# Performance work log

Measured on AMD Instinct MI355X. Metric: run time of the kernel, lower is better.

Reference implementation:

```python
import jax, jax.numpy as jnp
import numpy as np

N_NODES = 100000
N_EDGES = 1600000
IN_CH = 6
EDGE_FEAT = 8


def glorot(key, shape):
    lim = np.sqrt(6.0 / (shape[0] + shape[1]))
    return jax.random.uniform(key, shape, jnp.float32, -lim, lim)


def setup_inputs() -> dict:
    key = jax.random.key(0)
    ks = jax.random.split(key, 10)
    x = jax.random.normal(ks[0], (N_NODES, IN_CH), jnp.float32)
    edge_index = jax.random.randint(ks[1], (2, N_EDGES), 0, N_NODES, jnp.int64)
    edge_attr = jax.random.normal(ks[2], (N_EDGES, EDGE_FEAT), jnp.float32)
    return {
        "x": x,
        "edge_index": edge_index,
        "edge_attr": edge_attr,
        "W1": glorot(ks[3], (IN_CH, 32)), "b1": jnp.zeros((32,), jnp.float32),
        "W2": glorot(ks[4], (32, 16)), "b2": jnp.zeros((16,), jnp.float32),
        "W3": glorot(ks[5], (16 * 2 + EDGE_FEAT, 32)), "b3": jnp.zeros((32,), jnp.float32),
        "W4": glorot(ks[6], (32, 1)), "b4": jnp.zeros((1,), jnp.float32),
    }


def gcn_conv(x, src, dst, W, b, n_nodes):
    # PyG GCNConv: add self-loops, symmetric deg^{-1/2} normalization,
    # linear transform, scatter-add aggregation over incoming edges, bias.
    h = x @ W  # [N, out]
    deg = jnp.zeros((n_nodes,), h.dtype).at[dst].add(1.0) + 1.0  # +1 self-loop
    dinv = jax.lax.rsqrt(deg)  # [N]
    norm = dinv[src] * dinv[dst]  # [E]
    msg = h[src] * norm[:, None]  # gather + scale
    agg = jnp.zeros_like(h).at[dst].add(msg)
    agg = agg + h * (dinv * dinv)[:, None]  # self-loop term
    return agg + b


def reference(x, edge_index, edge_attr, W1, b1, W2, b2, W3, b3, W4, b4):
    src, dst = edge_index[0], edge_index[1]
    n = x.shape[0]
    h = jax.nn.relu(gcn_conv(x, src, dst, W1, b1, n))
    h = jax.nn.relu(gcn_conv(h, src, dst, W2, b2, n))
    # edge gather-concat-MLP
    edge_input = jnp.concatenate([h[src], h[dst], edge_attr], axis=1)  # [E, 40]
    out = jax.nn.relu(edge_input @ W3 + b3) @ W4 + b4  # [E, 1]
    return out.squeeze(-1)
```

## Files before the change

### kernel.cpp

```cpp
#include <hip/hip_runtime.h>


constexpr int TPB = 256;
constexpr int NB = 256;
constexpr int BSH = 8;
constexpr int MAXB = 1024;
constexpr int EDGE_ITERS = 8;

using short8  = __attribute__((ext_vector_type(8))) short;
using f32x4   = __attribute__((ext_vector_type(4))) float;
using uintx4  = __attribute__((ext_vector_type(4))) unsigned;
using floatx4 = __attribute__((ext_vector_type(4))) float;

__device__ __forceinline__ void nt_store4(uint4 v, uint4* p) {
    uintx4 e = {v.x, v.y, v.z, v.w};
    __builtin_nontemporal_store(e, reinterpret_cast<uintx4*>(p));
}
__device__ __forceinline__ float4 nt_load_f4(const float4* p) {
    floatx4 e = __builtin_nontemporal_load(reinterpret_cast<const floatx4*>(p));
    return float4{e.x, e.y, e.z, e.w};
}

__device__ __forceinline__ float bf_lo(unsigned w) {
    return __builtin_bit_cast(float, (unsigned)(w << 16));
}
__device__ __forceinline__ float bf_hi(unsigned w) {
    return __builtin_bit_cast(float, w & 0xFFFF0000u);
}
__device__ __forceinline__ unsigned bf1(float f) {
    unsigned u = __builtin_bit_cast(unsigned, f);
    return (u + 0x7FFFu + ((u >> 16) & 1u)) >> 16;
}
__device__ __forceinline__ unsigned pk(float lo, float hi) {
    return bf1(lo) | (bf1(hi) << 16);
}
__device__ __forceinline__ void unp8(uint4 v, float* o) {
    o[0] = bf_lo(v.x); o[1] = bf_hi(v.x); o[2] = bf_lo(v.y); o[3] = bf_hi(v.y);
    o[4] = bf_lo(v.z); o[5] = bf_hi(v.z); o[6] = bf_lo(v.w); o[7] = bf_hi(v.w);
}
__device__ __forceinline__ void unp6(uint4 v, float* o) {
    o[0] = bf_lo(v.x); o[1] = bf_hi(v.x); o[2] = bf_lo(v.y); o[3] = bf_hi(v.y);
    o[4] = bf_lo(v.z); o[5] = bf_hi(v.z);
}

__global__ void k_bhist(const int* __restrict__ dst, unsigned* __restrict__ histG,
                        int E, int B, int CH) {
    __shared__ unsigned h[MAXB];
    for (int t = threadIdx.x; t < B; t += blockDim.x) h[t] = 0;
    __syncthreads();
    int b = blockIdx.x;
    int beg = b * CH, end = min(E, beg + CH);
    for (int i = beg + threadIdx.x; i < end; i += blockDim.x)
        atomicAdd(&h[__builtin_nontemporal_load(dst + i) >> BSH], 1u);
    __syncthreads();
    for (int t = threadIdx.x; t < B; t += blockDim.x) histG[b * B + t] = h[t];
}

__global__ void k_scan1t(const unsigned* __restrict__ histG, unsigned* __restrict__ bsum,
                         int M, int B) {
    __shared__ unsigned s[TPB];
    int tid = threadIdx.x;
    int i = blockIdx.x * TPB + tid;
    unsigned v = (i < M) ? histG[(i % NB) * B + (i / NB)] : 0u;
    s[tid] = v;
    __syncthreads();
    for (int ofs = TPB / 2; ofs > 0; ofs >>= 1) {
        if (tid < ofs) s[tid] += s[tid + ofs];
        __syncthreads();
    }
    if (tid == 0) bsum[blockIdx.x] = s[0];
}

__global__ void k_scan2(unsigned* __restrict__ bsum, int nb) {
    __shared__ unsigned s[512];
    int tid = threadIdx.x;
    unsigned v = (tid < nb) ? bsum[tid] : 0u;
    s[tid] = v;
    __syncthreads();
    for (int ofs = 1; ofs < 512; ofs <<= 1) {
        unsigned t = (tid >= ofs) ? s[tid - ofs] : 0u;
        __syncthreads();
        s[tid] += t;
        __syncthreads();
    }
    if (tid < nb) bsum[tid] = s[tid] - v;
}

__global__ void k_scan3t(const unsigned* __restrict__ histG, const unsigned* __restrict__ bsum,
                         unsigned* __restrict__ scannedM, int M, int B) {
    __shared__ unsigned s[TPB];
    int tid = threadIdx.x;
    int i = blockIdx.x * TPB + tid;
    unsigned v = (i < M) ? histG[(i % NB) * B + (i / NB)] : 0u;
    s[tid] = v;
    __syncthreads();
    for (int ofs = 1; ofs < TPB; ofs <<= 1) {
        unsigned t = (tid >= ofs) ? s[tid - ofs] : 0u;
        __syncthreads();
        s[tid] += t;
        __syncthreads();
    }
    if (i < M) scannedM[i] = bsum[blockIdx.x] + s[tid] - v;
}

__global__ void k_bscatter(const int* __restrict__ src, const int* __restrict__ dst,
                           const unsigned* __restrict__ scannedM, unsigned* __restrict__ lvl1,
                           int E, int B, int CH) {
    __shared__ unsigned cur[MAXB];
    int b = blockIdx.x;
    for (int t = threadIdx.x; t < B; t += blockDim.x) cur[t] = scannedM[t * NB + b];
    __syncthreads();
    int beg = b * CH, end = min(E, beg + CH);
    for (int i = beg + threadIdx.x; i < end; i += blockDim.x) {
        int d = __builtin_nontemporal_load(dst + i);
        int sv = __builtin_nontemporal_load(src + i);
        int bk = d >> BSH;
        unsigned p = atomicAdd(&cur[bk], 1u);
        lvl1[p] = ((unsigned)sv << BSH) | (unsigned)(d & ((1 << BSH) - 1));
    }
}

__global__ void k_bbuild(const unsigned* __restrict__ lvl1, const unsigned* __restrict__ scannedM,
                         unsigned* __restrict__ rowptr, float* __restrict__ dinv,
                         int* __restrict__ csr_src, int N, int E, int B) {
    __shared__ unsigned cnt[1 << BSH];
    __shared__ unsigned ro[1 << BSH];
    int b = blockIdx.x;
    int tid = threadIdx.x;
    unsigned gbase = scannedM[(size_t)b * NB];
    unsigned gend = (b + 1 < B) ? scannedM[(size_t)(b + 1) * NB] : (unsigned)E;
    cnt[tid] = 0;
    __syncthreads();
    for (unsigned i = gbase + tid; i < gend; i += (unsigned)blockDim.x)
        atomicAdd(&cnt[lvl1[i] & ((1u << BSH) - 1u)], 1u);
    __syncthreads();
    unsigned v = cnt[tid];
    ro[tid] = v;
    __syncthreads();
    for (int ofs = 1; ofs < (1 << BSH); ofs <<= 1) {
        unsigned t = (tid >= ofs) ? ro[tid - ofs] : 0u;
        __syncthreads();
        ro[tid] += t;
        __syncthreads();
    }
    unsigned excl = ro[tid] - v;
    int n = (b << BSH) + tid;
    if (n < N) {
        rowptr[n] = gbase + excl;
        dinv[n] = rsqrtf((float)v + 1.0f);
        if (n == N - 1) rowptr[N] = gend;
    }
    __syncthreads();
    cnt[tid] = gbase + excl;
    __syncthreads();
    for (unsigned i = gbase + tid; i < gend; i += (unsigned)blockDim.x) {
        unsigned w = lvl1[i];
        unsigned p = atomicAdd(&cnt[w & ((1u << BSH) - 1u)], 1u);
        csr_src[p] = (int)(w >> BSH);
    }
}

__global__ void k_xs(const float* __restrict__ x, const float* __restrict__ dinv,
                     uint4* __restrict__ xs, int N) {
    int n = blockIdx.x * blockDim.x + threadIdx.x;
    if (n >= N) return;
    const float* xr = x + (size_t)n * 6;
    float di = dinv[n];
    uint4 o;
    o.x = pk(xr[0] * di, xr[1] * di);
    o.y = pk(xr[2] * di, xr[3] * di);
    o.z = pk(xr[4] * di, xr[5] * di);
    o.w = 0u;
    xs[n] = o;
}

__global__ void k_gagg6(const unsigned* __restrict__ rowptr, const int* __restrict__ csr_src,
                        const float* __restrict__ dinv, const uint4* __restrict__ xs,
                        const float* __restrict__ W1, const float* __restrict__ b1,
                        uint4* __restrict__ h1out, int N) {
    int gid = blockIdx.x * blockDim.x + threadIdx.x;
    int n = gid >> 2, q = gid & 3;
    if (n >= N) return;
    unsigned beg = rowptr[n], end = rowptr[n + 1];
    float acc[6] = {0.f, 0.f, 0.f, 0.f, 0.f, 0.f};
    for (unsigned j = beg + q; j < end; j += 4) {
        int s = __builtin_nontemporal_load(csr_src + j);
        float t[6];
        unp6(xs[s], t);
#pragma unroll
        for (int i = 0; i < 6; ++i) acc[i] += t[i];
    }
#pragma unroll
    for (int i = 0; i < 6; ++i) {
        acc[i] += __shfl_xor(acc[i], 1);
        acc[i] += __shfl_xor(acc[i], 2);
    }
    float t6[6];
    unp6(xs[n], t6);
#pragma unroll
    for (int i = 0; i < 6; ++i) acc[i] += t6[i];
    float di = dinv[n];
    unsigned w[4];
#pragma unroll
    for (int p = 0; p < 4; ++p) {
        int oc = q * 8 + 2 * p;
        float s0 = 0.f, s1 = 0.f;
#pragma unroll
        for (int k = 0; k < 6; ++k) {
            s0 = fmaf(acc[k], W1[k * 32 + oc], s0);
            s1 = fmaf(acc[k], W1[k * 32 + oc + 1], s1);
        }
        float r0 = fmaxf(fmaf(s0, di, b1[oc]), 0.f);
        float r1 = fmaxf(fmaf(s1, di, b1[oc + 1]), 0.f);
        w[p] = pk(r0, r1);
    }
    nt_store4(uint4{w[0], w[1], w[2], w[3]}, h1out + (size_t)n * 4 + q);
}

__global__ void k_lin2(const uint4* __restrict__ h1out, const float* __restrict__ W2,
                       const float* __restrict__ dinv, uint4* __restrict__ hs2, int N) {
    int gid = blockIdx.x * blockDim.x + threadIdx.x;
    if (gid >= N * 2) return;
    int n = gid >> 1, g = gid & 1;
    float h[32];
#pragma unroll
    for (int q = 0; q < 4; ++q) unp8(h1out[(size_t)n * 4 + q], h + q * 8);
    float di = dinv[n];
    unsigned w[4];
#pragma unroll
    for (int p = 0; p < 4; ++p) {
        int oc = g * 8 + 2 * p;
        float s0 = 0.f, s1 = 0.f;
#pragma unroll
        for (int c = 0; c < 32; ++c) {
            s0 = fmaf(h[c], W2[c * 16 + oc], s0);
            s1 = fmaf(h[c], W2[c * 16 + oc + 1], s1);
        }
        w[p] = pk(s0 * di, s1 * di);
    }
    nt_store4(uint4{w[0], w[1], w[2], w[3]}, hs2 + (size_t)n * 2 + g);
}

__global__ void k_gagg16(const unsigned* __restrict__ rowptr, const int* __restrict__ csr_src,
                         const float* __restrict__ dinv, const uint4* __restrict__ hs2,
                         const float* __restrict__ b2, uint4* __restrict__ h2, int N) {
    int gid = blockIdx.x * blockDim.x + threadIdx.x;
    int n = gid >> 2, q = gid & 3;
    int h = q & 1, e2 = q >> 1;
    if (n >= N) return;
    unsigned beg = rowptr[n], end = rowptr[n + 1];
    float acc[8] = {0.f, 0.f, 0.f, 0.f, 0.f, 0.f, 0.f, 0.f};
    for (unsigned j = beg + e2; j < end; j += 2) {
        int s = __builtin_nontemporal_load(csr_src + j);
        float t[8];
        unp8(hs2[(size_t)s * 2 + h], t);
#pragma unroll
        for (int i = 0; i < 8; ++i) acc[i] += t[i];
    }
#pragma unroll
    for (int i = 0; i < 8; ++i) acc[i] += __shfl_xor(acc[i], 2);
    if (e2) return;
    float t8[8];
    unp8(hs2[(size_t)n * 2 + h], t8);
    float di = dinv[n];
    unsigned w[4];
#pragma unroll
    for (int i = 0; i < 4; ++i) {
        float r0 = fmaxf(fmaf(acc[2 * i] + t8[2 * i], di, b2[h * 8 + 2 * i]), 0.f);
        float r1 = fmaxf(fmaf(acc[2 * i + 1] + t8[2 * i + 1], di, b2[h * 8 + 2 * i + 1]), 0.f);
        w[i] = pk(r0, r1);
    }
    h2[(size_t)n * 2 + h] = uint4{w[0], w[1], w[2], w[3]};
}

__global__ void k_wprep(const float* __restrict__ W3, const float* __restrict__ b3,
                        uint4* __restrict__ w3tab) {
    int lane = threadIdx.x;
    if (lane >= 64) return;
    int l15 = lane & 15, kb = lane >> 4;
    unsigned w0[2][4], w1[2][4];
#pragma unroll
    for (int t = 0; t < 2; ++t) {
#pragma unroll
        for (int p = 0; p < 4; ++p) {
            int k0 = kb * 8 + 2 * p;
            w0[t][p] = pk(W3[k0 * 32 + t * 16 + l15], W3[(k0 + 1) * 32 + t * 16 + l15]);
            int k1 = 32 + kb * 8 + 2 * p;
            float f0 = (k1 < 40) ? W3[k1 * 32 + t * 16 + l15]
                                 : (k1 == 40 ? b3[t * 16 + l15] : 0.f);
            float f1 = (k1 + 1 < 40) ? W3[(k1 + 1) * 32 + t * 16 + l15] : 0.f;
            w1[t][p] = pk(f0, f1);
        }
    }
    w3tab[lane * 4 + 0] = uint4{w0[0][0], w0[0][1], w0[0][2], w0[0][3]};
    w3tab[lane * 4 + 1] = uint4{w0[1][0], w0[1][1], w0[1][2], w0[1][3]};
    w3tab[lane * 4 + 2] = uint4{w1[0][0], w1[0][1], w1[0][2], w1[0][3]};
    w3tab[lane * 4 + 3] = uint4{w1[1][0], w1[1][1], w1[1][2], w1[1][3]};
}

__global__ void __launch_bounds__(TPB) k_edge_mfma(
    const int* __restrict__ src, const int* __restrict__ dst,
    const uint4* __restrict__ h2, const float* __restrict__ eattr,
    const uint4* __restrict__ w3tab, const float* __restrict__ W4,
    const float* __restrict__ b4, float* __restrict__ out, int E) {
    const int lane = threadIdx.x & 63;
    const int wave = threadIdx.x >> 6;
    const int l15 = lane & 15;
    const int kb = lane >> 4;

    short8 w3k0[2], w3k1[2];
    {
        const uint4* wt = w3tab + (size_t)lane * 4;
        w3k0[0] = __builtin_bit_cast(short8, wt[0]);
        w3k0[1] = __builtin_bit_cast(short8, wt[1]);
        w3k1[0] = __builtin_bit_cast(short8, wt[2]);
        w3k1[1] = __builtin_bit_cast(short8, wt[3]);
    }
    const float4 w4v0 = reinterpret_cast<const float4*>(W4)[kb];
    const float4 w4v1 = reinterpret_cast<const float4*>(W4)[4 + kb];
    const float b4v = b4[0];
    const int* idx_tab = (kb >= 2) ? dst : src;
    const long base0 = ((long)blockIdx.x * 4 + wave) * (16L * EDGE_ITERS);

    const uint4 one_u = (kb == 1) ? uint4{0x3F80u, 0u, 0u, 0u} : uint4{0u, 0u, 0u, 0u};
    const short8 one_s8 = __builtin_bit_cast(short8, one_u);

    auto eclamp = [&](int it) -> size_t {
        long et = base0 + (long)it * 16 + l15;
        return (size_t)(et < E ? et : (long)(E - 1));
    };
    auto load_a1 = [&](int it) -> short8 {
        if (kb != 0) return one_s8;
        const float4* ea = reinterpret_cast<const float4*>(eattr + eclamp(it) * 8);
        float4 e0 = nt_load_f4(ea);
        float4 e1 = nt_load_f4(ea + 1);
        return __builtin_bit_cast(short8, uint4{pk(e0.x, e0.y), pk(e0.z, e0.w),
                                                pk(e1.x, e1.y), pk(e1.z, e1.w)});
    };

    int idxA = __builtin_nontemporal_load(idx_tab + eclamp(0));
    int idxB = __builtin_nontemporal_load(idx_tab + eclamp(1));
    uint4 hvA = h2[(size_t)idxA * 2 + (kb & 1)];
    short8 a1A = load_a1(0);
    uint4 hvB = h2[(size_t)idxB * 2 + (kb & 1)];
    short8 a1B = load_a1(1);

#pragma unroll
    for (int it = 0; it < EDGE_ITERS; ++it) {
        uint4 hvC{0u, 0u, 0u, 0u};
        short8 a1C = one_s8;
        if (it + 2 < EDGE_ITERS) {
            int idxC = __builtin_nontemporal_load(idx_tab + eclamp(it + 2));
            hvC = h2[(size_t)idxC * 2 + (kb & 1)];
            a1C = load_a1(it + 2);
        }

        short8 a0 = __builtin_bit_cast(short8, hvA);
        f32x4 c0 = {0.f, 0.f, 0.f, 0.f}, c1 = {0.f, 0.f, 0.f, 0.f};
        c0 = __builtin_amdgcn_mfma_f32_16x16x32_bf16(w3k0[0], a0, c0, 0, 0, 0);
        c0 = __builtin_amdgcn_mfma_f32_16x16x32_bf16(w3k1[0], a1A, c0, 0, 0, 0);
        c1 = __builtin_amdgcn_mfma_f32_16x16x32_bf16(w3k0[1], a0, c1, 0, 0, 0);
        c1 = __builtin_amdgcn_mfma_f32_16x16x32_bf16(w3k1[1], a1A, c1, 0, 0, 0);

        float z = fmaxf(c0[0], 0.f) * w4v0.x;
        z = fmaf(fmaxf(c0[1], 0.f), w4v0.y, z);
        z = fmaf(fmaxf(c0[2], 0.f), w4v0.z, z);
        z = fmaf(fmaxf(c0[3], 0.f), w4v0.w, z);
        z = fmaf(fmaxf(c1[0], 0.f), w4v1.x, z);
        z = fmaf(fmaxf(c1[1], 0.f), w4v1.y, z);
        z = fmaf(fmaxf(c1[2], 0.f), w4v1.z, z);
        z = fmaf(fmaxf(c1[3], 0.f), w4v1.w, z);
        z += __shfl_xor(z, 16);
        z += __shfl_xor(z, 32);
        long erow = base0 + (long)it * 16 + l15;
        if (kb == 0 && erow < E) __builtin_nontemporal_store(z + b4v, out + erow);

        hvA = hvB; a1A = a1B;
        hvB = hvC; a1B = a1C;
    }
}

extern "C" void kernel_launch(void* const* d_in, const int* in_sizes, int n_in,
                              void* d_out, int out_size, void* d_ws, size_t ws_size,
                              hipStream_t stream) {
    const float* x     = (const float*)d_in[0];
    const int*   ei    = (const int*)d_in[1];
    const float* eattr = (const float*)d_in[2];
    const float* W1 = (const float*)d_in[3];
    const float* b1 = (const float*)d_in[4];
    const float* W2 = (const float*)d_in[5];
    const float* b2 = (const float*)d_in[6];
    const float* W3 = (const float*)d_in[7];
    const float* b3 = (const float*)d_in[8];
    const float* W4 = (const float*)d_in[9];
    const float* b4 = (const float*)d_in[10];
    float* out = (float*)d_out;

    const int N = in_sizes[0] / 6;
    const int E = in_sizes[2] / 8;
    const int* src = ei;
    const int* dst = ei + E;

    const int B  = (N + (1 << BSH) - 1) >> BSH;
    const int CH = (E + NB - 1) / NB;
    const int M  = B * NB;
    const int nbM = (M + TPB - 1) / TPB;

    char* wsb = (char*)d_ws;
    size_t off = 0;
    auto alloc4 = [&](size_t elems) {
        void* p = wsb + off;
        off += ((elems * 4 + 15) & ~(size_t)15);
        return p;
    };
    unsigned* rowptr   = (unsigned*)alloc4(N + 1);
    float*    dinv     = (float*)alloc4(N);
    unsigned* bsum     = (unsigned*)alloc4(512);
    unsigned* histG    = (unsigned*)alloc4((size_t)NB * B);
    unsigned* scannedM = (unsigned*)alloc4((size_t)NB * B);
    int*      csr_src  = (int*)alloc4(E);
    unsigned* big      = (unsigned*)alloc4((size_t)N * 16 > (size_t)E ? (size_t)N * 16 : (size_t)E);
    uint4*    h1out    = (uint4*)alloc4((size_t)N * 16);
    uint4*    xs       = (uint4*)alloc4((size_t)N * 4);
    uint4*    w3tab    = (uint4*)alloc4(64 * 4 * 4);

    unsigned* lvl1 = big;
    uint4*    hs2  = (uint4*)big;
    uint4*    h2   = (uint4*)(big + (size_t)N * 8);

    k_wprep<<<1, 64, 0, stream>>>(W3, b3, w3tab);

    k_bhist   <<<NB, TPB, 0, stream>>>(dst, histG, E, B, CH);
    k_scan1t  <<<nbM, TPB, 0, stream>>>(histG, bsum, M, B);
    k_scan2   <<<1, 512, 0, stream>>>(bsum, nbM);
    k_scan3t  <<<nbM, TPB, 0, stream>>>(histG, bsum, scannedM, M, B);
    k_bscatter<<<NB, TPB, 0, stream>>>(src, dst, scannedM, lvl1, E, B, CH);
    k_bbuild  <<<B, 1 << BSH, 0, stream>>>(lvl1, scannedM, rowptr, dinv, csr_src, N, E, B);

    const int nbN = (N + TPB - 1) / TPB;
    k_xs   <<<nbN, TPB, 0, stream>>>(x, dinv, xs, N);
    k_gagg6<<<((size_t)N * 4 + TPB - 1) / TPB, TPB, 0, stream>>>(
        rowptr, csr_src, dinv, xs, W1, b1, h1out, N);

    k_lin2  <<<(N * 2 + TPB - 1) / TPB, TPB, 0, stream>>>(h1out, W2, dinv, hs2, N);
    k_gagg16<<<((size_t)N * 4 + TPB - 1) / TPB, TPB, 0, stream>>>(
        rowptr, csr_src, dinv, hs2, b2, h2, N);

    const long per_block = 4L * 16 * EDGE_ITERS;
    const int eblocks = (int)((E + per_block - 1) / per_block);
    k_edge_mfma<<<eblocks, TPB, 0, stream>>>(src, dst, (const uint4*)h2, eattr,
                                             (const uint4*)w3tab, W4, b4, out, E);
}
```

Before: 175.0 us.

## Fuse xs into CSR build, fuse layer-1 linear with W2, widen aggregation

Computes the dinv-scaled bf16 node features inside k_bbuild, which removes the k_xs launch. Fuses the W1 transform, ReLU and W2 projection into the first aggregation kernel, with a shuffle reduction across the four lanes, so the k_lin2 launch and the h1out round trip are gone. Spreads the second aggregation over 8 threads per node instead of 4 to raise memory parallelism. Halves EDGE_ITERS in the edge MLP and preloads all edge indices up front, giving more blocks with less work each.

```diff
diff --git a/kernel.cpp b/kernel.cpp
--- a/kernel.cpp
+++ b/kernel.cpp
@@ -5,7 +5,7 @@
 constexpr int NB = 256;
 constexpr int BSH = 8;
 constexpr int MAXB = 1024;
-constexpr int EDGE_ITERS = 8;
+constexpr int EDGE_ITERS = 4;
 
 using short8  = __attribute__((ext_vector_type(8))) short;
 using f32x4   = __attribute__((ext_vector_type(4))) float;
@@ -121,7 +121,8 @@
 }
 
 __global__ void k_bbuild(const unsigned* __restrict__ lvl1, const unsigned* __restrict__ scannedM,
-                         unsigned* __restrict__ rowptr, float* __restrict__ dinv,
+                         const float* __restrict__ x, unsigned* __restrict__ rowptr,
+                         float* __restrict__ dinv, uint4* __restrict__ xs,
                          int* __restrict__ csr_src, int N, int E, int B) {
     __shared__ unsigned cnt[1 << BSH];
     __shared__ unsigned ro[1 << BSH];
@@ -147,7 +148,15 @@
     int n = (b << BSH) + tid;
     if (n < N) {
         rowptr[n] = gbase + excl;
-        dinv[n] = rsqrtf((float)v + 1.0f);
+        float di = rsqrtf((float)v + 1.0f);
+        dinv[n] = di;
+        const float* xr = x + (size_t)n * 6;
+        uint4 o;
+        o.x = pk(xr[0] * di, xr[1] * di);
+        o.y = pk(xr[2] * di, xr[3] * di);
+        o.z = pk(xr[4] * di, xr[5] * di);
+        o.w = 0u;
+        xs[n] = o;
         if (n == N - 1) rowptr[N] = gend;
     }
     __syncthreads();
@@ -160,24 +169,10 @@
     }
 }
 
-__global__ void k_xs(const float* __restrict__ x, const float* __restrict__ dinv,
-                     uint4* __restrict__ xs, int N) {
-    int n = blockIdx.x * blockDim.x + threadIdx.x;
-    if (n >= N) return;
-    const float* xr = x + (size_t)n * 6;
-    float di = dinv[n];
-    uint4 o;
-    o.x = pk(xr[0] * di, xr[1] * di);
-    o.y = pk(xr[2] * di, xr[3] * di);
-    o.z = pk(xr[4] * di, xr[5] * di);
-    o.w = 0u;
-    xs[n] = o;
-}
-
-__global__ void k_gagg6(const unsigned* __restrict__ rowptr, const int* __restrict__ csr_src,
-                        const float* __restrict__ dinv, const uint4* __restrict__ xs,
-                        const float* __restrict__ W1, const float* __restrict__ b1,
-                        uint4* __restrict__ h1out, int N) {
+__global__ void k_gagg6f(const unsigned* __restrict__ rowptr, const int* __restrict__ csr_src,
+                         const float* __restrict__ dinv, const uint4* __restrict__ xs,
+                         const float* __restrict__ W1, const float* __restrict__ b1,
+                         const float* __restrict__ W2, uint4* __restrict__ hs2, int N) {
     int gid = blockIdx.x * blockDim.x + threadIdx.x;
     int n = gid >> 2, q = gid & 3;
     if (n >= N) return;
@@ -200,57 +195,49 @@
 #pragma unroll
     for (int i = 0; i < 6; ++i) acc[i] += t6[i];
     float di = dinv[n];
-    unsigned w[4];
-#pragma unroll
-    for (int p = 0; p < 4; ++p) {
-        int oc = q * 8 + 2 * p;
-        float s0 = 0.f, s1 = 0.f;
-#pragma unroll
-        for (int k = 0; k < 6; ++k) {
-            s0 = fmaf(acc[k], W1[k * 32 + oc], s0);
-            s1 = fmaf(acc[k], W1[k * 32 + oc + 1], s1);
-        }
-        float r0 = fmaxf(fmaf(s0, di, b1[oc]), 0.f);
-        float r1 = fmaxf(fmaf(s1, di, b1[oc + 1]), 0.f);
-        w[p] = pk(r0, r1);
-    }
-    nt_store4(uint4{w[0], w[1], w[2], w[3]}, h1out + (size_t)n * 4 + q);
-}
-
-__global__ void k_lin2(const uint4* __restrict__ h1out, const float* __restrict__ W2,
-                       const float* __restrict__ dinv, uint4* __restrict__ hs2, int N) {
-    int gid = blockIdx.x * blockDim.x + threadIdx.x;
-    if (gid >= N * 2) return;
-    int n = gid >> 1, g = gid & 1;
-    float h[32];
-#pragma unroll
-    for (int q = 0; q < 4; ++q) unp8(h1out[(size_t)n * 4 + q], h + q * 8);
-    float di = dinv[n];
-    unsigned w[4];
-#pragma unroll
-    for (int p = 0; p < 4; ++p) {
-        int oc = g * 8 + 2 * p;
-        float s0 = 0.f, s1 = 0.f;
-#pragma unroll
-        for (int c = 0; c < 32; ++c) {
-            s0 = fmaf(h[c], W2[c * 16 + oc], s0);
-            s1 = fmaf(h[c], W2[c * 16 + oc + 1], s1);
-        }
-        w[p] = pk(s0 * di, s1 * di);
-    }
-    nt_store4(uint4{w[0], w[1], w[2], w[3]}, hs2 + (size_t)n * 2 + g);
+    float h1[8];
+#pragma unroll
+    for (int cc = 0; cc < 8; ++cc) {
+        int oc = q * 8 + cc;
+        float s = 0.f;
+#pragma unroll
+        for (int k = 0; k < 6; ++k) s = fmaf(acc[k], W1[k * 32 + oc], s);
+        h1[cc] = fmaxf(fmaf(s, di, b1[oc]), 0.f);
+    }
+    float z[16];
+#pragma unroll
+    for (int j = 0; j < 16; ++j) z[j] = 0.f;
+#pragma unroll
+    for (int cc = 0; cc < 8; ++cc) {
+        int c = q * 8 + cc;
+        float a = h1[cc];
+#pragma unroll
+        for (int j = 0; j < 16; ++j) z[j] = fmaf(a, W2[c * 16 + j], z[j]);
+    }
+#pragma unroll
+    for (int j = 0; j < 16; ++j) {
+        z[j] += __shfl_xor(z[j], 1);
+        z[j] += __shfl_xor(z[j], 2);
+    }
+    if (q < 2) {
+        unsigned w[4];
+#pragma unroll
+        for (int p = 0; p < 4; ++p)
+            w[p] = pk(z[q * 8 + 2 * p] * di, z[q * 8 + 2 * p + 1] * di);
+        nt_store4(uint4{w[0], w[1], w[2], w[3]}, hs2 + (size_t)n * 2 + q);
+    }
 }
 
 __global__ void k_gagg16(const unsigned* __restrict__ rowptr, const int* __restrict__ csr_src,
                          const float* __restrict__ dinv, const uint4* __restrict__ hs2,
                          const float* __restrict__ b2, uint4* __restrict__ h2, int N) {
     int gid = blockIdx.x * blockDim.x + threadIdx.x;
-    int n = gid >> 2, q = gid & 3;
-    int h = q & 1, e2 = q >> 1;
+    int n = gid >> 3, q = gid & 7;
+    int h = q & 1, e4 = q >> 1;
     if (n >= N) return;
     unsigned beg = rowptr[n], end = rowptr[n + 1];
     float acc[8] = {0.f, 0.f, 0.f, 0.f, 0.f, 0.f, 0.f, 0.f};
-    for (unsigned j = beg + e2; j < end; j += 2) {
+    for (unsigned j = beg + e4; j < end; j += 4) {
         int s = __builtin_nontemporal_load(csr_src + j);
         float t[8];
         unp8(hs2[(size_t)s * 2 + h], t);
@@ -258,8 +245,11 @@
         for (int i = 0; i < 8; ++i) acc[i] += t[i];
     }
 #pragma unroll
-    for (int i = 0; i < 8; ++i) acc[i] += __shfl_xor(acc[i], 2);
-    if (e2) return;
+    for (int i = 0; i < 8; ++i) {
+        acc[i] += __shfl_xor(acc[i], 2);
+        acc[i] += __shfl_xor(acc[i], 4);
+    }
+    if (e4) return;
     float t8[8];
     unp8(hs2[(size_t)n * 2 + h], t8);
     float di = dinv[n];
@@ -338,11 +328,14 @@
                                                 pk(e1.x, e1.y), pk(e1.z, e1.w)});
     };
 
-    int idxA = __builtin_nontemporal_load(idx_tab + eclamp(0));
-    int idxB = __builtin_nontemporal_load(idx_tab + eclamp(1));
-    uint4 hvA = h2[(size_t)idxA * 2 + (kb & 1)];
+    int idx[EDGE_ITERS];
+#pragma unroll
+    for (int it = 0; it < EDGE_ITERS; ++it)
+        idx[it] = __builtin_nontemporal_load(idx_tab + eclamp(it));
+
+    uint4 hvA = h2[(size_t)idx[0] * 2 + (kb & 1)];
     short8 a1A = load_a1(0);
-    uint4 hvB = h2[(size_t)idxB * 2 + (kb & 1)];
+    uint4 hvB = h2[(size_t)idx[1] * 2 + (kb & 1)];
     short8 a1B = load_a1(1);
 
 #pragma unroll
@@ -350,8 +343,7 @@
         uint4 hvC{0u, 0u, 0u, 0u};
         short8 a1C = one_s8;
         if (it + 2 < EDGE_ITERS) {
-            int idxC = __builtin_nontemporal_load(idx_tab + eclamp(it + 2));
-            hvC = h2[(size_t)idxC * 2 + (kb & 1)];
+            hvC = h2[(size_t)idx[it + 2] * 2 + (kb & 1)];
             a1C = load_a1(it + 2);
         }
 
@@ -420,7 +412,6 @@
     unsigned* scannedM = (unsigned*)alloc4((size_t)NB * B);
     int*      csr_src  = (int*)alloc4(E);
     unsigned* big      = (unsigned*)alloc4((size_t)N * 16 > (size_t)E ? (size_t)N * 16 : (size_t)E);
-    uint4*    h1out    = (uint4*)alloc4((size_t)N * 16);
     uint4*    xs       = (uint4*)alloc4((size_t)N * 4);
     uint4*    w3tab    = (uint4*)alloc4(64 * 4 * 4);
 
@@ -435,15 +426,12 @@
     k_scan2   <<<1, 512, 0, stream>>>(bsum, nbM);
     k_scan3t  <<<nbM, TPB, 0, stream>>>(histG, bsum, scannedM, M, B);
     k_bscatter<<<NB, TPB, 0, stream>>>(src, dst, scannedM, lvl1, E, B, CH);
-    k_bbuild  <<<B, 1 << BSH, 0, stream>>>(lvl1, scannedM, rowptr, dinv, csr_src, N, E, B);
-
-    const int nbN = (N + TPB - 1) / TPB;
-    k_xs   <<<nbN, TPB, 0, stream>>>(x, dinv, xs, N);
-    k_gagg6<<<((size_t)N * 4 + TPB - 1) / TPB, TPB, 0, stream>>>(
-        rowptr, csr_src, dinv, xs, W1, b1, h1out, N);
-
-    k_lin2  <<<(N * 2 + TPB - 1) / TPB, TPB, 0, stream>>>(h1out, W2, dinv, hs2, N);
-    k_gagg16<<<((size_t)N * 4 + TPB - 1) / TPB, TPB, 0, stream>>>(
+    k_bbuild  <<<B, 1 << BSH, 0, stream>>>(lvl1, scannedM, x, rowptr, dinv, xs, csr_src, N, E, B);
+
+    k_gagg6f<<<((size_t)N * 4 + TPB - 1) / TPB, TPB, 0, stream>>>(
+        rowptr, csr_src, dinv, xs, W1, b1, W2, hs2, N);
+
+    k_gagg16<<<((size_t)N * 8 + TPB - 1) / TPB, TPB, 0, stream>>>(
         rowptr, csr_src, dinv, hs2, b2, h2, N);
 
     const long per_block = 4L * 16 * EDGE_ITERS;
```

New measurement: 178.2 us. About the same (+1.9%).
